# Performance work log

Hardware: AMD Instinct MI355X
Metric: run time of the kernel (lower is better)

## Reference

```python
import jax, jax.numpy as jnp
import numpy as np

MASK_THRED = 1        # init kwarg mask_thred
TRIPLE_WEIGHT = 1.0   # init kwarg triple_weight (scales gradient of shifted branch)
NEG = -1e30
EPS = 1e-8


def setup_inputs() -> dict:
    key = jax.random.key(0)
    k1, k2 = jax.random.split(key)
    x = jax.random.normal(k1, (2, 128, 96, 96), dtype=jnp.float32)
    mask = jax.random.randint(k2, (96, 96), 0, 2, dtype=jnp.int32)
    return {"x": x, "mask": mask}


def reference(x, mask):
    # x: (B, C, H, W); former = x[:, :C//2], latter = x[:, C//2:]
    B, C, H, W = x.shape
    c2 = C // 2
    hw = H * W

    # shift_sz=1, stride=1, mask_thred=1 -> a location is 'masked' iff mask >= 1
    flag = mask.reshape(hw) >= MASK_THRED  # (hw,) True = inside hole

    former, latter = x[:, :c2], x[:, c2:]

    # similarity path is non-differentiable in the original (hard argmax, detached latter)
    lat = jax.lax.stop_gradient(latter).reshape(B, c2, hw).transpose(0, 2, 1)  # (B, hw, c2)
    # original normalizes only the candidate (non-masked) patches (NCC filters)
    lat_n = lat / jnp.maximum(jnp.linalg.norm(lat, axis=-1, keepdims=True), EPS)

    # cross-correlation of every location against every (normalized) candidate
    sim = jnp.einsum('bic,bjc->bij', lat, lat_n)  # (B, hw, hw)
    # only non-masked locations are valid candidates j
    sim = jnp.where(flag[None, None, :], NEG, sim)
    idx = jnp.argmax(sim, axis=-1)  # (B, hw) nearest non-masked neighbor per location

    # shift: copy the FORMER feature from the matched non-masked location
    fmr = former.reshape(B, c2, hw).transpose(0, 2, 1)  # (B, hw, c2)
    gathered = jnp.take_along_axis(fmr, idx[:, :, None], axis=1)  # (B, hw, c2)

    # triple_weight scales only the gradient of the shifted branch (fwd unchanged)
    tw = jnp.float32(TRIPLE_WEIGHT)
    gathered = gathered * tw + jax.lax.stop_gradient(gathered * (1.0 - tw))

    # shifted features only at masked locations, zero elsewhere
    shift = jnp.where(flag[None, :, None], gathered, jnp.float32(0.0))
    shift = shift.transpose(0, 2, 1).reshape(B, c2, H, W)

    # triple: (former, latter, shifted) -> (B, 3*C//2, H, W)
    return jnp.concatenate([former, latter, shift], axis=1)
```

## Files before the change

### kernel.cpp

```cpp
#include <hip/hip_runtime.h>
#include <math.h>

#define HW 9216
#define NSTRIP 288
#define NCH 18
#define NCOPY 160
#define EPSN 1e-8f

typedef _Float16 f16x8  __attribute__((ext_vector_type(8)));
typedef float    f32x16 __attribute__((ext_vector_type(16)));

__global__ __launch_bounds__(256) void prep_kernel(
    const float* __restrict__ x, const float4* __restrict__ x4,
    const int* __restrict__ mask,
    int* __restrict__ ilist, int* __restrict__ jlist, int* __restrict__ counts,
    _Float16* __restrict__ aH, _Float16* __restrict__ aL,
    _Float16* __restrict__ bH, _Float16* __restrict__ bL,
    unsigned long long* __restrict__ amax, float4* __restrict__ out4)
{
    __shared__ unsigned short slot16[HW];
    __shared__ int wsum[4];
    int tid = threadIdx.x;
    if (blockIdx.x >= 288) {
        const int N = 128 * (HW / 4);
        for (int e = (blockIdx.x - 288) * 256 + tid; e < 2 * N; e += NCOPY * 256) {
            int b = e / N, rem = e - b * N;
            out4[(size_t)b * 192 * (HW / 4) + rem] = x4[(size_t)b * N + rem];
        }
        return;
    }
    int base = tid * 36;
    const int4* mp4 = (const int4*)mask + tid * 9;
    unsigned long long fl = 0ull; int cnt = 0;
#pragma unroll
    for (int k4 = 0; k4 < 9; k4++) {
        int4 m4 = mp4[k4];
        int f0 = (m4.x >= 1), f1 = (m4.y >= 1), f2 = (m4.z >= 1), f3 = (m4.w >= 1);
        fl |= ((unsigned long long)f0 << (k4 * 4)) | ((unsigned long long)f1 << (k4 * 4 + 1)) |
              ((unsigned long long)f2 << (k4 * 4 + 2)) | ((unsigned long long)f3 << (k4 * 4 + 3));
        cnt += f0 + f1 + f2 + f3;
    }
    int lane = tid & 63, wave = tid >> 6;
    int v = cnt;
#pragma unroll
    for (int off = 1; off < 64; off <<= 1) {
        int u = __shfl_up(v, off, 64);
        if (lane >= off) v += u;
    }
    if (lane == 63) wsum[wave] = v;
    __syncthreads();
    int woff = 0;
#pragma unroll
    for (int w = 0; w < 4; w++) if (w < wave) woff += wsum[w];
    int incl = v + woff;
    int excl = incl - cnt;
    int posF = excl, posU = base - excl;
    bool wl = (blockIdx.x == 0);
#pragma unroll
    for (int k = 0; k < 36; k++) {
        int p = base + k;
        if ((fl >> k) & 1ull) { slot16[p] = (unsigned short)(posF | 0x8000); if (wl) ilist[posF] = p; posF++; }
        else                  { slot16[p] = (unsigned short)posU;            if (wl) jlist[posU] = p; posU++; }
    }
    if (wl && tid == 255) { counts[0] = incl; counts[1] = HW - incl; }
    __syncthreads();
    int t = blockIdx.x * 256 + tid;
    int sub = t & 63;
    int q = sub >> 4;
    int pb = ((t >> 6) << 4) | (sub & 15);
    int b = pb / HW, p = pb - b * HW;
    const float* xl = x + (size_t)(b * 128 + 64) * HW + p;
    float vv[16]; float ss = 0.f;
#pragma unroll
    for (int e = 0; e < 16; e++) { float w0 = xl[(size_t)(q * 16 + e) * HW]; vv[e] = w0; ss = fmaf(w0, w0, ss); }
    ss += __shfl_xor(ss, 16, 64);
    ss += __shfl_xor(ss, 32, 64);
    float inv = 1.0f / fmaxf(sqrtf(ss), EPSN);
    if (q == 0) amax[pb] = 0ull;
    unsigned sl = slot16[p];
    int flagged = sl >> 15;
    int slot = sl & 0x7fff;
    float scale = flagged ? 1.0f : inv;
    int tile = slot >> 5, lnp = slot & 31;
    _Float16* dh = flagged ? aH : bH;
    _Float16* dl = flagged ? aL : bL;
#pragma unroll
    for (int h = 0; h < 2; h++) {
        size_t off = ((((size_t)b * NSTRIP + tile) * 4 + q) * 64 + h * 32 + lnp) * 8;
        f16x8 hh, ll;
#pragma unroll
        for (int e = 0; e < 8; e++) {
            float w0 = vv[h * 8 + e] * scale;
            _Float16 hv = (_Float16)w0;
            hh[e] = hv; ll[e] = (_Float16)((w0 - (float)hv) * 2048.0f);
        }
        *(f16x8*)(dh + off) = hh; *(f16x8*)(dl + off) = ll;
    }
}

__device__ __forceinline__ unsigned int ordf(float f) {
    unsigned int u = __float_as_uint(f);
    return (u & 0x80000000u) ? ~u : (u | 0x80000000u);
}

__global__ __launch_bounds__(256, 2) void argmax_kernel(
    const _Float16* __restrict__ aH, const _Float16* __restrict__ aL,
    const _Float16* __restrict__ bH, const _Float16* __restrict__ bL,
    const int* __restrict__ ilist, const int* __restrict__ counts,
    unsigned long long* __restrict__ amax)
{
    int ni = counts[0];
    if (blockIdx.x * 256 >= ni) return;
    int nj = counts[1];
    int njt = (nj + 31) >> 5;
    int tpc = (njt + NCH - 1) / NCH;
    int s = blockIdx.y;
    int jt0 = s * tpc, jt1 = min(jt0 + tpc, njt);
    if (jt0 >= jt1) return;
    int b = blockIdx.z;
    int wave = threadIdx.x >> 6, l = threadIdx.x & 63;
    int base = (blockIdx.x * 4 + wave) * 64;
    int g = l >> 5, ln = l & 31;
    int strip0 = base >> 5;

    __shared__ f16x8 lds[2][8][64];

    const f16x8* apH = (const f16x8*)aH + ((size_t)b * NSTRIP + strip0) * 256 + l;
    const f16x8* apL = (const f16x8*)aL + ((size_t)b * NSTRIP + strip0) * 256 + l;
    f16x8 xh0 = apH[0],   xh1 = apH[64],  xh2 = apH[128], xh3 = apH[192];
    f16x8 xl0 = apL[0],   xl1 = apL[64],  xl2 = apL[128], xl3 = apL[192];
    f16x8 yh0 = apH[256], yh1 = apH[320], yh2 = apH[384], yh3 = apH[448];
    f16x8 yl0 = apL[256], yl1 = apL[320], yl2 = apL[384], yl3 = apL[448];

    int f0 = wave * 2;
    const f16x8* s0 = (const f16x8*)((f0 < 4) ? bH : bL) +
                      (size_t)b * NSTRIP * 256 + (size_t)(f0 & 3) * 64 + l;
    const f16x8* s1 = (const f16x8*)((f0 + 1 < 4) ? bH : bL) +
                      (size_t)b * NSTRIP * 256 + (size_t)((f0 + 1) & 3) * 64 + l;

    {
        f16x8 t0 = s0[(size_t)jt0 * 256];
        f16x8 t1 = s1[(size_t)jt0 * 256];
        lds[0][f0][l] = t0;
        lds[0][f0 + 1][l] = t1;
    }
    __syncthreads();

    float bv0 = -INFINITY, bv1 = -INFINITY;
    int bj0 = -1, bj1 = -1;
    int cur = 0;

    for (int jt = jt0; jt < jt1; ++jt, cur ^= 1) {
        f16x8 n0, n1;
        bool more = (jt + 1 < jt1);
        if (more) {
            n0 = s0[(size_t)(jt + 1) * 256];
            n1 = s1[(size_t)(jt + 1) * 256];
        }
        f16x8 bh0 = lds[cur][0][l], bh1 = lds[cur][1][l];
        f16x8 bh2 = lds[cur][2][l], bh3 = lds[cur][3][l];
        f16x8 bl0 = lds[cur][4][l], bl1 = lds[cur][5][l];
        f16x8 bl2 = lds[cur][6][l], bl3 = lds[cur][7][l];
        f32x16 cH0 = {}, cC0 = {}, cH1 = {}, cC1 = {};
        cH0 = __builtin_amdgcn_mfma_f32_32x32x16_f16(bh0, xh0, cH0, 0, 0, 0);
        cC0 = __builtin_amdgcn_mfma_f32_32x32x16_f16(bh0, xl0, cC0, 0, 0, 0);
        cC0 = __builtin_amdgcn_mfma_f32_32x32x16_f16(bl0, xh0, cC0, 0, 0, 0);
        cH0 = __builtin_amdgcn_mfma_f32_32x32x16_f16(bh1, xh1, cH0, 0, 0, 0);
        cC0 = __builtin_amdgcn_mfma_f32_32x32x16_f16(bh1, xl1, cC0, 0, 0, 0);
        cC0 = __builtin_amdgcn_mfma_f32_32x32x16_f16(bl1, xh1, cC0, 0, 0, 0);
        cH0 = __builtin_amdgcn_mfma_f32_32x32x16_f16(bh2, xh2, cH0, 0, 0, 0);
        cC0 = __builtin_amdgcn_mfma_f32_32x32x16_f16(bh2, xl2, cC0, 0, 0, 0);
        cC0 = __builtin_amdgcn_mfma_f32_32x32x16_f16(bl2, xh2, cC0, 0, 0, 0);
        cH0 = __builtin_amdgcn_mfma_f32_32x32x16_f16(bh3, xh3, cH0, 0, 0, 0);
        cC0 = __builtin_amdgcn_mfma_f32_32x32x16_f16(bh3, xl3, cC0, 0, 0, 0);
        cC0 = __builtin_amdgcn_mfma_f32_32x32x16_f16(bl3, xh3, cC0, 0, 0, 0);
        cH1 = __builtin_amdgcn_mfma_f32_32x32x16_f16(bh0, yh0, cH1, 0, 0, 0);
        cC1 = __builtin_amdgcn_mfma_f32_32x32x16_f16(bh0, yl0, cC1, 0, 0, 0);
        cC1 = __builtin_amdgcn_mfma_f32_32x32x16_f16(bl0, yh0, cC1, 0, 0, 0);
        cH1 = __builtin_amdgcn_mfma_f32_32x32x16_f16(bh1, yh1, cH1, 0, 0, 0);
        cC1 = __builtin_amdgcn_mfma_f32_32x32x16_f16(bh1, yl1, cC1, 0, 0, 0);
        cC1 = __builtin_amdgcn_mfma_f32_32x32x16_f16(bl1, yh1, cC1, 0, 0, 0);
        cH1 = __builtin_amdgcn_mfma_f32_32x32x16_f16(bh2, yh2, cH1, 0, 0, 0);
        cC1 = __builtin_amdgcn_mfma_f32_32x32x16_f16(bh2, yl2, cC1, 0, 0, 0);
        cC1 = __builtin_amdgcn_mfma_f32_32x32x16_f16(bl2, yh2, cC1, 0, 0, 0);
        cH1 = __builtin_amdgcn_mfma_f32_32x32x16_f16(bh3, yh3, cH1, 0, 0, 0);
        cC1 = __builtin_amdgcn_mfma_f32_32x32x16_f16(bh3, yl3, cC1, 0, 0, 0);
        cC1 = __builtin_amdgcn_mfma_f32_32x32x16_f16(bl3, yh3, cC1, 0, 0, 0);
        int jb = jt << 5;
        if (jb + 32 <= nj) {
#pragma unroll
            for (int r = 0; r < 16; ++r) {
                int row = (r & 3) + 8 * (r >> 2) + 4 * g;
                int j = jb + row;
                float v0 = fmaf(cC0[r], 4.8828125e-4f , cH0[r]);
                float v1 = fmaf(cC1[r], 4.8828125e-4f, cH1[r]);
                if (v0 > bv0) { bv0 = v0; bj0 = j; }
                if (v1 > bv1) { bv1 = v1; bj1 = j; }
            }
        } else {
#pragma unroll
            for (int r = 0; r < 16; ++r) {
                int row = (r & 3) + 8 * (r >> 2) + 4 * g;
                int j = jb + row;
                float v0 = fmaf(cC0[r], 4.8828125e-4f, cH0[r]);
                float v1 = fmaf(cC1[r], 4.8828125e-4f, cH1[r]);
                if (j < nj && v0 > bv0) { bv0 = v0; bj0 = j; }
                if (j < nj && v1 > bv1) { bv1 = v1; bj1 = j; }
            }
        }
        if (more) {
            lds[cur ^ 1][f0][l] = n0;
            lds[cur ^ 1][f0 + 1][l] = n1;
        }
        __syncthreads();
    }

    unsigned long long k0 = ((unsigned long long)ordf(bv0) << 32) |
                            (unsigned long long)(~(unsigned int)bj0);
    unsigned long long k1 = ((unsigned long long)ordf(bv1) << 32) |
                            (unsigned long long)(~(unsigned int)bj1);
    unsigned long long o0 = __shfl_xor(k0, 32, 64);
    unsigned long long o1 = __shfl_xor(k1, 32, 64);
    if (o0 > k0) k0 = o0;
    if (o1 > k1) k1 = o1;
    int il0 = base + ln, il1 = base + 32 + ln;
    if (g == 0) {
        if (il0 < ni && (unsigned)(k0 >> 32) > 0x007FFFFFu)
            atomicMax(&amax[(size_t)b * HW + ilist[il0]], k0);
        if (il1 < ni && (unsigned)(k1 >> 32) > 0x007FFFFFu)
            atomicMax(&amax[(size_t)b * HW + ilist[il1]], k1);
    }
}

__global__ void epilogue_kernel(const float* __restrict__ x,
                                const int* __restrict__ mask,
                                const unsigned long long* __restrict__ amax,
                                const int* __restrict__ jlist, float4* __restrict__ out4) {
    const int q = HW / 4;
    int t = blockIdx.x * blockDim.x + threadIdx.x;
    if (t >= 2 * 64 * q) return;
    int pos4 = t % q;
    int cs = (t / q) % 64;
    int b = t / (64 * q);
    float4 v = make_float4(0.f, 0.f, 0.f, 0.f);
    float* vp = &v.x;
    int pos = pos4 * 4;
    const float* xf = x + (size_t)(b * 128 + cs) * HW;
#pragma unroll
    for (int k = 0; k < 4; k++) {
        int p = pos + k;
        if (mask[p] >= 1) {
            unsigned long long key = amax[(size_t)b * HW + p];
            int j = 0;
            if (key != 0ull) j = jlist[(int)(~(unsigned int)key)];
            vp[k] = xf[j];
        }
    }
    out4[((size_t)b * 192 + 128 + cs) * q + pos4] = v;
}

extern "C" void kernel_launch(void* const* d_in, const int* in_sizes, int n_in,
                              void* d_out, int out_size, void* d_ws, size_t ws_size,
                              hipStream_t stream) {
    const float* x = (const float*)d_in[0];
    const int* mask = (const int*)d_in[1];
    float4* out4 = (float4*)d_out;

    char* ws = (char*)d_ws;
    int*   counts = (int*)ws;
    int*   ilist  = (int*)(ws + 128);
    int*   jlist  = (int*)(ws + 36992);
    unsigned long long* amax = (unsigned long long*)(ws + 73856);
    _Float16* aH = (_Float16*)(ws + 221312);
    _Float16* aL = (_Float16*)(ws + 221312 + 1 * 2359296);
    _Float16* bH = (_Float16*)(ws + 221312 + 2 * 2359296);
    _Float16* bL = (_Float16*)(ws + 221312 + 3 * 2359296);

    prep_kernel<<<288 + NCOPY, 256, 0, stream>>>(x, (const float4*)x, mask,
                                                 ilist, jlist, counts,
                                                 aH, aL, bH, bL, amax, out4);
    {
        dim3 grid(NSTRIP / 8, NCH, 2);
        argmax_kernel<<<grid, 256, 0, stream>>>(aH, aL, bH, bL, ilist, counts, amax);
    }
    {
        int n = 2 * 64 * (HW / 4);
        epilogue_kernel<<<(n + 255) / 256, 256, 0, stream>>>(x, mask, amax, jlist, out4);
    }
}
```

Measured before the change: 97.91 us.

## Fuse prep, argmax and epilogue into one cooperative persistent kernel with grid syncs

Merges the three kernels into a single cooperative launch that uses grid.sync() between the prep/copy phase, the argmax phase and the epilogue. The goal is to remove the gaps between kernel launches and to size the argmax chunk count (nch) to the persistent grid. The old three-kernel path stays as a fallback when occupancy is too low or the cooperative launch fails. Costs include two grid-wide barriers, a grid capped at 768 blocks, and a launch bound of 3 blocks per CU that may limit registers for argmax.

Result: no change. 98.53 us (+0.6%).

```diff
diff --git a/kernel.cpp b/kernel.cpp
--- a/kernel.cpp
+++ b/kernel.cpp
@@ -1,34 +1,27 @@
 #include <hip/hip_runtime.h>
+#include <hip/hip_cooperative_groups.h>
 #include <math.h>
+
+namespace cg = cooperative_groups;
 
 #define HW 9216
 #define NSTRIP 288
-#define NCH 18
+#define NCH_CLASSIC 18
 #define NCOPY 160
 #define EPSN 1e-8f
 
 typedef _Float16 f16x8  __attribute__((ext_vector_type(8)));
 typedef float    f32x16 __attribute__((ext_vector_type(16)));
 
-__global__ __launch_bounds__(256) void prep_kernel(
-    const float* __restrict__ x, const float4* __restrict__ x4,
-    const int* __restrict__ mask,
+
+__device__ __forceinline__ void prep_compute(
+    int bid, int tid, unsigned short* slot16, int* wsum,
+    const float* __restrict__ x, const int* __restrict__ mask,
     int* __restrict__ ilist, int* __restrict__ jlist, int* __restrict__ counts,
     _Float16* __restrict__ aH, _Float16* __restrict__ aL,
     _Float16* __restrict__ bH, _Float16* __restrict__ bL,
-    unsigned long long* __restrict__ amax, float4* __restrict__ out4)
-{
-    __shared__ unsigned short slot16[HW];
-    __shared__ int wsum[4];
-    int tid = threadIdx.x;
-    if (blockIdx.x >= 288) {
-        const int N = 128 * (HW / 4);
-        for (int e = (blockIdx.x - 288) * 256 + tid; e < 2 * N; e += NCOPY * 256) {
-            int b = e / N, rem = e - b * N;
-            out4[(size_t)b * 192 * (HW / 4) + rem] = x4[(size_t)b * N + rem];
-        }
-        return;
-    }
+    unsigned long long* __restrict__ amax)
+{
     int base = tid * 36;
     const int4* mp4 = (const int4*)mask + tid * 9;
     unsigned long long fl = 0ull; int cnt = 0;
@@ -55,7 +48,7 @@
     int incl = v + woff;
     int excl = incl - cnt;
     int posF = excl, posU = base - excl;
-    bool wl = (blockIdx.x == 0);
+    bool wl = (bid == 0);
 #pragma unroll
     for (int k = 0; k < 36; k++) {
         int p = base + k;
@@ -64,19 +57,19 @@
     }
     if (wl && tid == 255) { counts[0] = incl; counts[1] = HW - incl; }
     __syncthreads();
-    int t = blockIdx.x * 256 + tid;
+    int t = bid * 256 + tid;
     int sub = t & 63;
-    int q = sub >> 4;
+    int cq = sub >> 4;
     int pb = ((t >> 6) << 4) | (sub & 15);
     int b = pb / HW, p = pb - b * HW;
     const float* xl = x + (size_t)(b * 128 + 64) * HW + p;
     float vv[16]; float ss = 0.f;
 #pragma unroll
-    for (int e = 0; e < 16; e++) { float w0 = xl[(size_t)(q * 16 + e) * HW]; vv[e] = w0; ss = fmaf(w0, w0, ss); }
+    for (int e = 0; e < 16; e++) { float w0 = xl[(size_t)(cq * 16 + e) * HW]; vv[e] = w0; ss = fmaf(w0, w0, ss); }
     ss += __shfl_xor(ss, 16, 64);
     ss += __shfl_xor(ss, 32, 64);
     float inv = 1.0f / fmaxf(sqrtf(ss), EPSN);
-    if (q == 0) amax[pb] = 0ull;
+    if (cq == 0) amax[pb] = 0ull;
     unsigned sl = slot16[p];
     int flagged = sl >> 15;
     int slot = sl & 0x7fff;
@@ -86,7 +79,7 @@
     _Float16* dl = flagged ? aL : bL;
 #pragma unroll
     for (int h = 0; h < 2; h++) {
-        size_t off = ((((size_t)b * NSTRIP + tile) * 4 + q) * 64 + h * 32 + lnp) * 8;
+        size_t off = ((((size_t)b * NSTRIP + tile) * 4 + cq) * 64 + h * 32 + lnp) * 8;
         f16x8 hh, ll;
 #pragma unroll
         for (int e = 0; e < 8; e++) {
@@ -98,32 +91,36 @@
     }
 }
 
+__device__ __forceinline__ void copy_body(int cbid, int tid, int ncopy,
+    const float4* __restrict__ x4, float4* __restrict__ out4)
+{
+    const int N = 128 * (HW / 4);
+    for (int e = cbid * 256 + tid; e < 2 * N; e += ncopy * 256) {
+        int b = e / N, rem = e - b * N;
+        out4[(size_t)b * 192 * (HW / 4) + rem] = x4[(size_t)b * N + rem];
+    }
+}
+
 __device__ __forceinline__ unsigned int ordf(float f) {
     unsigned int u = __float_as_uint(f);
     return (u & 0x80000000u) ? ~u : (u | 0x80000000u);
 }
 
-__global__ __launch_bounds__(256, 2) void argmax_kernel(
+__device__ __forceinline__ void argmax_item(
+    int ig, int s, int b, int nch, int ni, int nj, int tid,
+    f16x8 (*lds)[8][64],
     const _Float16* __restrict__ aH, const _Float16* __restrict__ aL,
     const _Float16* __restrict__ bH, const _Float16* __restrict__ bL,
-    const int* __restrict__ ilist, const int* __restrict__ counts,
-    unsigned long long* __restrict__ amax)
-{
-    int ni = counts[0];
-    if (blockIdx.x * 256 >= ni) return;
-    int nj = counts[1];
+    const int* __restrict__ ilist, unsigned long long* __restrict__ amax)
+{
     int njt = (nj + 31) >> 5;
-    int tpc = (njt + NCH - 1) / NCH;
-    int s = blockIdx.y;
+    int tpc = (njt + nch - 1) / nch;
     int jt0 = s * tpc, jt1 = min(jt0 + tpc, njt);
     if (jt0 >= jt1) return;
-    int b = blockIdx.z;
-    int wave = threadIdx.x >> 6, l = threadIdx.x & 63;
-    int base = (blockIdx.x * 4 + wave) * 64;
+    int wave = tid >> 6, l = tid & 63;
+    int base = (ig * 4 + wave) * 64;
     int g = l >> 5, ln = l & 31;
     int strip0 = base >> 5;
-
-    __shared__ f16x8 lds[2][8][64];
 
     const f16x8* apH = (const f16x8*)aH + ((size_t)b * NSTRIP + strip0) * 256 + l;
     const f16x8* apL = (const f16x8*)aL + ((size_t)b * NSTRIP + strip0) * 256 + l;
@@ -232,13 +229,12 @@
     }
 }
 
-__global__ void epilogue_kernel(const float* __restrict__ x,
-                                const int* __restrict__ mask,
-                                const unsigned long long* __restrict__ amax,
-                                const int* __restrict__ jlist, float4* __restrict__ out4) {
+__device__ __forceinline__ void epilogue_elem(int t,
+    const float* __restrict__ x, const int* __restrict__ mask,
+    const unsigned long long* __restrict__ amax, const int* __restrict__ jlist,
+    float4* __restrict__ out4)
+{
     const int q = HW / 4;
-    int t = blockIdx.x * blockDim.x + threadIdx.x;
-    if (t >= 2 * 64 * q) return;
     int pos4 = t % q;
     int cs = (t / q) % 64;
     int b = t / (64 * q);
@@ -257,6 +253,82 @@
         }
     }
     out4[((size_t)b * 192 + 128 + cs) * q + pos4] = v;
+}
+
+__global__ __launch_bounds__(256, 3) void fused_kernel(
+    const float* __restrict__ x, const float4* __restrict__ x4,
+    const int* __restrict__ mask,
+    int* __restrict__ ilist, int* __restrict__ jlist, int* __restrict__ counts,
+    _Float16* __restrict__ aH, _Float16* __restrict__ aL,
+    _Float16* __restrict__ bH, _Float16* __restrict__ bL,
+    unsigned long long* __restrict__ amax, float4* __restrict__ out4, int nch)
+{
+    __shared__ __align__(16) char smem[18448];
+    cg::grid_group grid = cg::this_grid();
+    int bid = blockIdx.x, tid = threadIdx.x;
+    if (bid < 288) {
+        prep_compute(bid, tid, (unsigned short*)smem, (int*)(smem + 18432),
+                     x, mask, ilist, jlist, counts, aH, aL, bH, bL, amax);
+    } else {
+        copy_body(bid - 288, tid, (int)gridDim.x - 288, x4, out4);
+    }
+    grid.sync();
+    {
+        int ni = counts[0], nj = counts[1];
+        int nig = (ni + 255) >> 8;
+        int total = nig * nch * 2;
+        for (int item = bid; item < total; item += (int)gridDim.x) {
+            int ig = item % nig;
+            int rest = item / nig;
+            int s = rest % nch;
+            int b = rest / nch;
+            argmax_item(ig, s, b, nch, ni, nj, tid,
+                        reinterpret_cast<f16x8 (*)[8][64]>(smem),
+                        aH, aL, bH, bL, ilist, amax);
+        }
+    }
+    grid.sync();
+    {
+        const int n = 2 * 64 * (HW / 4);
+        for (int t = bid * 256 + tid; t < n; t += (int)gridDim.x * 256)
+            epilogue_elem(t, x, mask, amax, jlist, out4);
+    }
+}
+
+__global__ __launch_bounds__(256) void prep_kernel(
+    const float* __restrict__ x, const float4* __restrict__ x4,
+    const int* __restrict__ mask,
+    int* __restrict__ ilist, int* __restrict__ jlist, int* __restrict__ counts,
+    _Float16* __restrict__ aH, _Float16* __restrict__ aL,
+    _Float16* __restrict__ bH, _Float16* __restrict__ bL,
+    unsigned long long* __restrict__ amax, float4* __restrict__ out4)
+{
+    __shared__ __align__(16) char smem[18448];
+    if (blockIdx.x >= 288) { copy_body(blockIdx.x - 288, threadIdx.x, NCOPY, x4, out4); return; }
+    prep_compute(blockIdx.x, threadIdx.x, (unsigned short*)smem, (int*)(smem + 18432),
+                 x, mask, ilist, jlist, counts, aH, aL, bH, bL, amax);
+}
+
+__global__ __launch_bounds__(256, 2) void argmax_kernel(
+    const _Float16* __restrict__ aH, const _Float16* __restrict__ aL,
+    const _Float16* __restrict__ bH, const _Float16* __restrict__ bL,
+    const int* __restrict__ ilist, const int* __restrict__ counts,
+    unsigned long long* __restrict__ amax)
+{
+    __shared__ __align__(16) f16x8 lds[2][8][64];
+    int ni = counts[0];
+    if (blockIdx.x * 256 >= ni) return;
+    argmax_item(blockIdx.x, blockIdx.y, blockIdx.z, NCH_CLASSIC, ni, counts[1],
+                threadIdx.x, lds, aH, aL, bH, bL, ilist, amax);
+}
+
+__global__ void epilogue_kernel(const float* __restrict__ x,
+                                const int* __restrict__ mask,
+                                const unsigned long long* __restrict__ amax,
+                                const int* __restrict__ jlist, float4* __restrict__ out4) {
+    int t = blockIdx.x * blockDim.x + threadIdx.x;
+    if (t >= 2 * 64 * (HW / 4)) return;
+    epilogue_elem(t, x, mask, amax, jlist, out4);
 }
 
 extern "C" void kernel_launch(void* const* d_in, const int* in_sizes, int n_in,
@@ -275,12 +347,33 @@
     _Float16* aL = (_Float16*)(ws + 221312 + 1 * 2359296);
     _Float16* bH = (_Float16*)(ws + 221312 + 2 * 2359296);
     _Float16* bL = (_Float16*)(ws + 221312 + 3 * 2359296);
-
-    prep_kernel<<<288 + NCOPY, 256, 0, stream>>>(x, (const float4*)x, mask,
-                                                 ilist, jlist, counts,
+    const float4* x4 = (const float4*)x;
+
+    static int coopGrid = -2;
+    if (coopGrid == -2) {
+        int nb = 0;
+        hipError_t e = hipOccupancyMaxActiveBlocksPerMultiprocessor(
+            &nb, (const void*)fused_kernel, 256, 0);
+        coopGrid = (e == hipSuccess && nb >= 2) ? ((nb * 256 > 768) ? 768 : nb * 256) : -1;
+    }
+
+    if (coopGrid >= 512) {
+        int nch = coopGrid / 36; if (nch > 21) nch = 21;
+        void* args[] = { (void*)&x, (void*)&x4, (void*)&mask,
+                         (void*)&ilist, (void*)&jlist, (void*)&counts,
+                         (void*)&aH, (void*)&aL, (void*)&bH, (void*)&bL,
+                         (void*)&amax, (void*)&out4, (void*)&nch };
+        hipError_t e = hipLaunchCooperativeKernel((const void*)fused_kernel,
+                                                  dim3(coopGrid), dim3(256),
+                                                  args, 0, stream);
+        if (e == hipSuccess) return;
+        coopGrid = -1;
+    }
+
+    prep_kernel<<<288 + NCOPY, 256, 0, stream>>>(x, x4, mask, ilist, jlist, counts,
                                                  aH, aL, bH, bL, amax, out4);
     {
-        dim3 grid(NSTRIP / 8, NCH, 2);
+        dim3 grid(NSTRIP / 8, NCH_CLASSIC, 2);
         argmax_kernel<<<grid, 256, 0, stream>>>(aH, aL, bH, bL, ilist, counts, amax);
     }
     {
```
